# Kernel optimization log

Hardware: AMD Instinct MI355X
Metric: run time of the kernel (lower is better)

The kernel has to match this reference:

```python
import jax, jax.numpy as jnp
import numpy as np

B, N_PER_GRAPH, DEG = 4, 50000, 32
NUM_RELS, NUM_BASES, N_LAYERS = 8, 4, 2
E_PER = N_PER_GRAPH * DEG
N_TOTAL = B * N_PER_GRAPH
E_TOTAL = B * E_PER


def setup_inputs() -> dict:
    key = jax.random.key(0)
    ks = jax.random.split(key, 10)
    # Block-structured edges: each graph's edges stay within its node block (dgl.batch semantics)
    src_b = jax.random.randint(ks[0], (B, E_PER), 0, N_PER_GRAPH)
    dst_b = jax.random.randint(ks[1], (B, E_PER), 0, N_PER_GRAPH)
    off = (jnp.arange(B) * N_PER_GRAPH)[:, None]
    src = (src_b + off).reshape(-1).astype(jnp.int64)
    dst = (dst_b + off).reshape(-1).astype(jnp.int64)
    edge_type = jax.random.randint(ks[2], (E_TOTAL,), 0, NUM_RELS).astype(jnp.int64)
    norm = jax.random.uniform(ks[3], (E_TOTAL, 1), dtype=jnp.float32)
    feat1 = jax.random.normal(ks[4], (N_TOTAL, 1), dtype=jnp.float32)
    feat2 = jax.random.normal(ks[5], (N_TOTAL, 1), dtype=jnp.float32)
    # RGCN basis-decomposition params per layer (in=out=h_dim=1)
    bases = jax.random.normal(ks[6], (N_LAYERS, NUM_BASES, 1, 1), dtype=jnp.float32) * 0.1
    w_comp = jax.random.normal(ks[7], (N_LAYERS, NUM_RELS, NUM_BASES), dtype=jnp.float32) * 0.1
    biases = jnp.zeros((N_LAYERS, 1), dtype=jnp.float32)  # DGL RelGraphConv bias (out_dim=1)
    W_lin = jax.random.normal(ks[8], (1024, N_PER_GRAPH), dtype=jnp.float32) / np.float32(np.sqrt(N_PER_GRAPH))
    b_lin = jnp.zeros((1024,), dtype=jnp.float32)
    return dict(feat1=feat1, feat2=feat2, src=src, dst=dst, edge_type=edge_type,
                norm=norm, num_nodes=N_PER_GRAPH, bases=bases, w_comp=w_comp,
                biases=biases, W_lin=W_lin, b_lin=b_lin)


def _forward_each(feat, src, dst, edge_type, norm, bases, w_comp, biases, W_lin, b_lin, num_nodes):
    n_total = feat.shape[0]
    n_layers = w_comp.shape[0]
    initial = feat
    x = feat
    for l in range(n_layers):
        # basis decomposition: per-relation (1x1) weight -> scalar per relation
        weight = (w_comp[l] @ bases[l].reshape(NUM_BASES, 1))  # (num_rels, 1)
        msg = x[src] * weight[edge_type] * norm               # (E, 1) gather + edge-wise transform
        agg = jax.ops.segment_sum(msg, dst, num_segments=n_total)  # scatter-sum per node
        h = agg + biases[l]
        if l < n_layers - 1:
            h = jax.nn.relu(h)
        x = h + initial  # residual add (x += initial)
    x = x.reshape(-1, num_nodes)          # (B, num_nodes) since h_dim == 1
    return x @ W_lin.T + b_lin            # (B, 1024)


def reference(feat1, feat2, src, dst, edge_type, norm, num_nodes, bases, w_comp, biases, W_lin, b_lin):
    x1 = _forward_each(feat1, src, dst, edge_type, norm, bases, w_comp, biases, W_lin, b_lin, num_nodes)
    x2 = _forward_each(feat2, src, dst, edge_type, norm, bases, w_comp, biases, W_lin, b_lin, num_nodes)
    x = jnp.sum(x1 * x2, axis=1, keepdims=True)  # (B, 1)
    return jax.nn.sigmoid(x)
```

## Files before the change

### kernel.cpp

```cpp
#include <hip/hip_runtime.h>
#include <hip/hip_bf16.h>
#include <math.h>

#define BB 4
#define N_PER 50000
#define DEG 32
#define NUM_RELS 8
#define NUM_BASES 4
#define N_LAYERS 2
#define E_PER (N_PER * DEG)
#define E_TOTAL (BB * E_PER)
#define N_TOTAL (BB * N_PER)
#define OUT_F 1024

#define RANGES 4
#define RANGE_SZ (N_PER / RANGES)
#define SUBS 16
#define EDGES_PER_BLOCK (E_PER / SUBS)
#define GROUPS_PER_BLOCK (EDGES_PER_BLOCK / 4)
#define PARTIAL_STRIDE (2 * RANGE_SZ)
#define NBLOCKS (BB * RANGES * SUBS)

#define GR 8
#define GKSPLIT 10
#define GKCHUNK (N_PER / GKSPLIT)
#define GROWBLKS (OUT_F / GR)
#define GEMV_BLOCKS (GROWBLKS * GKSPLIT)


__global__ __launch_bounds__(256) void init_kernel(
    const float* __restrict__ feat1, const float* __restrict__ feat2,
    const float* __restrict__ bases, const float* __restrict__ w_comp,
    float* __restrict__ ws) {
  int tid = blockIdx.x * blockDim.x + threadIdx.x;
  if (blockIdx.x == 0 && threadIdx.x < 16) {
    int l = threadIdx.x >> 3, r = threadIdx.x & 7;
    float s = 0.f;
#pragma unroll
    for (int b = 0; b < NUM_BASES; ++b)
      s += w_comp[l * NUM_RELS * NUM_BASES + r * NUM_BASES + b] *
           bases[l * NUM_BASES + b];
    ws[l * 8 + r] = s;
  }
  float* x1 = ws + 32;
  float* x2 = x1 + N_TOTAL;
  for (int i = tid; i < N_TOTAL; i += gridDim.x * blockDim.x) {
    x1[i] = feat1[i];
    x2[i] = feat2[i];
  }
}

__global__ __launch_bounds__(1024) void edge_bin_kernel(
    const int* __restrict__ src, const int* __restrict__ dst,
    const int* __restrict__ et, const float* __restrict__ norm,
    const float* __restrict__ relw, int layer,
    const float* __restrict__ x1, const float* __restrict__ x2,
    float* __restrict__ partials) {
  __shared__ float w[NUM_RELS];
  __shared__ float bin1[RANGE_SZ];
  __shared__ float bin2[RANGE_SZ];
  int bid = blockIdx.x;
  int sub = bid & (SUBS - 1);
  int br = bid >> 4;
  int b = br >> 2, r = br & 3;
  if (threadIdx.x < NUM_RELS) w[threadIdx.x] = relw[layer * 8 + threadIdx.x];
  for (int i = threadIdx.x; i < RANGE_SZ; i += blockDim.x) {
    bin1[i] = 0.f;
    bin2[i] = 0.f;
  }
  __syncthreads();

  int base = b * E_PER + sub * EDGES_PER_BLOCK;
  int node_lo = b * N_PER + r * RANGE_SZ;
  for (int g = threadIdx.x; g < GROUPS_PER_BLOCK; g += blockDim.x) {
    int e = base + g * 4;
    int4 s4 = *(const int4*)(src + e);
    int4 d4 = *(const int4*)(dst + e);
    int4 t4 = *(const int4*)(et + e);
    float4 n4 = *(const float4*)(norm + e);
    {
      int lr = d4.x - node_lo;
      if (lr >= 0 && lr < RANGE_SZ) {
        float c = w[t4.x] * n4.x;
        atomicAdd(&bin1[lr], x1[s4.x] * c);
        atomicAdd(&bin2[lr], x2[s4.x] * c);
      }
    }
    {
      int lr = d4.y - node_lo;
      if (lr >= 0 && lr < RANGE_SZ) {
        float c = w[t4.y] * n4.y;
        atomicAdd(&bin1[lr], x1[s4.y] * c);
        atomicAdd(&bin2[lr], x2[s4.y] * c);
      }
    }
    {
      int lr = d4.z - node_lo;
      if (lr >= 0 && lr < RANGE_SZ) {
        float c = w[t4.z] * n4.z;
        atomicAdd(&bin1[lr], x1[s4.z] * c);
        atomicAdd(&bin2[lr], x2[s4.z] * c);
      }
    }
    {
      int lr = d4.w - node_lo;
      if (lr >= 0 && lr < RANGE_SZ) {
        float c = w[t4.w] * n4.w;
        atomicAdd(&bin1[lr], x1[s4.w] * c);
        atomicAdd(&bin2[lr], x2[s4.w] * c);
      }
    }
  }
  __syncthreads();

  float* outp = partials + (size_t)bid * PARTIAL_STRIDE;
  for (int i = threadIdx.x; i < RANGE_SZ; i += blockDim.x) {
    outp[i] = bin1[i];
    outp[RANGE_SZ + i] = bin2[i];
  }
}

__global__ __launch_bounds__(256) void merge_node_kernel(
    const float* __restrict__ partials,
    const float* __restrict__ feat1, const float* __restrict__ feat2,
    const float* __restrict__ biases, int layer,
    float* __restrict__ x1, float* __restrict__ x2) {
  int i = blockIdx.x * 256 + threadIdx.x;
  if (i >= N_TOTAL) return;
  int b = i / N_PER;
  int local = i - b * N_PER;
  int r = local / RANGE_SZ;
  int lidx = local - r * RANGE_SZ;
  int blk0 = (b * RANGES + r) * SUBS;
  float s1 = 0.f, s2 = 0.f;
#pragma unroll
  for (int s = 0; s < SUBS; ++s) {
    const float* p = partials + (size_t)(blk0 + s) * PARTIAL_STRIDE;
    s1 += p[lidx];
    s2 += p[RANGE_SZ + lidx];
  }
  float bias = biases[layer];
  float h1 = s1 + bias, h2 = s2 + bias;
  if (layer < N_LAYERS - 1) {
    h1 = fmaxf(h1, 0.f);
    h2 = fmaxf(h2, 0.f);
  }
  x1[i] = h1 + feat1[i];
  x2[i] = h2 + feat2[i];
}

__global__ __launch_bounds__(256) void gemv_part_kernel(
    const float* __restrict__ W,
    const float* __restrict__ x1, const float* __restrict__ x2,
    float* __restrict__ gpart) {
  int bid = blockIdx.x;
  int rb = bid & (GROWBLKS - 1);
  int ks = bid >> 7;
  int j0 = rb * GR;
  int k0 = ks * GKCHUNK;

  float acc[GR][8];
#pragma unroll
  for (int r = 0; r < GR; ++r)
#pragma unroll
    for (int g = 0; g < 8; ++g) acc[r][g] = 0.f;

  for (int k = k0 + threadIdx.x * 4; k < k0 + GKCHUNK; k += 256 * 4) {
    float4 xv[8];
#pragma unroll
    for (int i = 0; i < 4; ++i) {
      xv[2 * i] = *(const float4*)(x1 + i * N_PER + k);
      xv[2 * i + 1] = *(const float4*)(x2 + i * N_PER + k);
    }
#pragma unroll
    for (int r = 0; r < GR; ++r) {
      float4 wv = *(const float4*)(W + (size_t)(j0 + r) * N_PER + k);
#pragma unroll
      for (int g = 0; g < 8; ++g) {
        acc[r][g] += wv.x * xv[g].x + wv.y * xv[g].y +
                     wv.z * xv[g].z + wv.w * xv[g].w;
      }
    }
  }

#pragma unroll
  for (int off = 32; off > 0; off >>= 1)
#pragma unroll
    for (int r = 0; r < GR; ++r)
#pragma unroll
      for (int g = 0; g < 8; ++g) acc[r][g] += __shfl_down(acc[r][g], off);

  __shared__ float red[4][GR * 8];
  int wave = threadIdx.x >> 6, lane = threadIdx.x & 63;
  if (lane == 0) {
#pragma unroll
    for (int r = 0; r < GR; ++r)
#pragma unroll
      for (int g = 0; g < 8; ++g) red[wave][r * 8 + g] = acc[r][g];
  }
  __syncthreads();
  if (threadIdx.x < GR * 8) {
    float s = red[0][threadIdx.x] + red[1][threadIdx.x] +
              red[2][threadIdx.x] + red[3][threadIdx.x];
    gpart[(size_t)bid * (GR * 8) + threadIdx.x] = s;
  }
}

__global__ __launch_bounds__(1024) void gemv_reduce_kernel(
    const float* __restrict__ gpart, const float* __restrict__ b_lin,
    float* __restrict__ out) {
  int j = threadIdx.x;
  int rb = j >> 3, rr = j & 7;
  float y[8];
#pragma unroll
  for (int g = 0; g < 8; ++g) y[g] = 0.f;
#pragma unroll
  for (int ks = 0; ks < GKSPLIT; ++ks) {
    const float* p = gpart + (size_t)(ks * GROWBLKS + rb) * (GR * 8) + rr * 8;
#pragma unroll
    for (int g = 0; g < 8; ++g) y[g] += p[g];
  }
  float bl = b_lin[j];
  float prod[4];
#pragma unroll
  for (int i = 0; i < 4; ++i)
    prod[i] = (y[2 * i] + bl) * (y[2 * i + 1] + bl);

#pragma unroll
  for (int off = 32; off > 0; off >>= 1)
#pragma unroll
    for (int i = 0; i < 4; ++i) prod[i] += __shfl_down(prod[i], off);

  __shared__ float red[16][4];
  int wave = threadIdx.x >> 6, lane = threadIdx.x & 63;
  if (lane == 0) {
#pragma unroll
    for (int i = 0; i < 4; ++i) red[wave][i] = prod[i];
  }
  __syncthreads();
  if (threadIdx.x < 4) {
    float s = 0.f;
#pragma unroll
    for (int wv = 0; wv < 16; ++wv) s += red[wv][threadIdx.x];
    out[threadIdx.x] = 1.f / (1.f + expf(-s));
  }
}

extern "C" void kernel_launch(void* const* d_in, const int* in_sizes, int n_in,
                              void* d_out, int out_size, void* d_ws, size_t ws_size,
                              hipStream_t stream) {
  const float* feat1 = (const float*)d_in[0];
  const float* feat2 = (const float*)d_in[1];
  const int* src = (const int*)d_in[2];
  const int* dst = (const int*)d_in[3];
  const int* et = (const int*)d_in[4];
  const float* norm = (const float*)d_in[5];
  const float* bases = (const float*)d_in[7];
  const float* w_comp = (const float*)d_in[8];
  const float* biases = (const float*)d_in[9];
  const float* W_lin = (const float*)d_in[10];
  const float* b_lin = (const float*)d_in[11];
  float* out = (float*)d_out;

  float* ws = (float*)d_ws;
  float* relw = ws;
  float* x1 = ws + 32;
  float* x2 = x1 + N_TOTAL;
  float* partials = x2 + N_TOTAL;

  int nblk = (N_TOTAL + 255) / 256;
  init_kernel<<<nblk, 256, 0, stream>>>(feat1, feat2, bases, w_comp, ws);

  for (int l = 0; l < N_LAYERS; ++l) {
    edge_bin_kernel<<<NBLOCKS, 1024, 0, stream>>>(src, dst, et, norm, relw, l,
                                                  x1, x2, partials);
    merge_node_kernel<<<nblk, 256, 0, stream>>>(partials, feat1, feat2, biases,
                                                l, x1, x2);
  }

  float* gpart = partials;
  gemv_part_kernel<<<GEMV_BLOCKS, 256, 0, stream>>>(W_lin, x1, x2, gpart);
  gemv_reduce_kernel<<<1, 1024, 0, stream>>>(gpart, b_lin, out);
}
```

Baseline: 554.9 us.

## Interleave the two feature streams and reorder edge-bin block mapping

```diff
diff --git a/kernel.cpp b/kernel.cpp
--- a/kernel.cpp
+++ b/kernel.cpp
@@ -42,11 +42,9 @@
            bases[l * NUM_BASES + b];
     ws[l * 8 + r] = s;
   }
-  float* x1 = ws + 32;
-  float* x2 = x1 + N_TOTAL;
+  float* x12 = ws + 32;
   for (int i = tid; i < N_TOTAL; i += gridDim.x * blockDim.x) {
-    x1[i] = feat1[i];
-    x2[i] = feat2[i];
+    *(float2*)(x12 + 2 * (size_t)i) = make_float2(feat1[i], feat2[i]);
   }
 }
 
@@ -54,20 +52,16 @@
     const int* __restrict__ src, const int* __restrict__ dst,
     const int* __restrict__ et, const float* __restrict__ norm,
     const float* __restrict__ relw, int layer,
-    const float* __restrict__ x1, const float* __restrict__ x2,
-    float* __restrict__ partials) {
+    const float* __restrict__ x12, float* __restrict__ partials) {
   __shared__ float w[NUM_RELS];
-  __shared__ float bin1[RANGE_SZ];
-  __shared__ float bin2[RANGE_SZ];
+  __shared__ float bin[2 * RANGE_SZ];
   int bid = blockIdx.x;
-  int sub = bid & (SUBS - 1);
-  int br = bid >> 4;
-  int b = br >> 2, r = br & 3;
+  int r = bid >> 6;
+  int pair = bid & 63;
+  int b = pair >> 4;
+  int sub = pair & 15;
   if (threadIdx.x < NUM_RELS) w[threadIdx.x] = relw[layer * 8 + threadIdx.x];
-  for (int i = threadIdx.x; i < RANGE_SZ; i += blockDim.x) {
-    bin1[i] = 0.f;
-    bin2[i] = 0.f;
-  }
+  for (int i = threadIdx.x; i < 2 * RANGE_SZ; i += blockDim.x) bin[i] = 0.f;
   __syncthreads();
 
   int base = b * E_PER + sub * EDGES_PER_BLOCK;
@@ -80,51 +74,54 @@
     float4 n4 = *(const float4*)(norm + e);
     {
       int lr = d4.x - node_lo;
-      if (lr >= 0 && lr < RANGE_SZ) {
+      if ((unsigned)lr < RANGE_SZ) {
+        float2 xv = *(const float2*)(x12 + 2 * (size_t)s4.x);
         float c = w[t4.x] * n4.x;
-        atomicAdd(&bin1[lr], x1[s4.x] * c);
-        atomicAdd(&bin2[lr], x2[s4.x] * c);
+        atomicAdd(&bin[2 * lr], xv.x * c);
+        atomicAdd(&bin[2 * lr + 1], xv.y * c);
       }
     }
     {
       int lr = d4.y - node_lo;
-      if (lr >= 0 && lr < RANGE_SZ) {
+      if ((unsigned)lr < RANGE_SZ) {
+        float2 xv = *(const float2*)(x12 + 2 * (size_t)s4.y);
         float c = w[t4.y] * n4.y;
-        atomicAdd(&bin1[lr], x1[s4.y] * c);
-        atomicAdd(&bin2[lr], x2[s4.y] * c);
+        atomicAdd(&bin[2 * lr], xv.x * c);
+        atomicAdd(&bin[2 * lr + 1], xv.y * c);
       }
     }
     {
       int lr = d4.z - node_lo;
-      if (lr >= 0 && lr < RANGE_SZ) {
+      if ((unsigned)lr < RANGE_SZ) {
+        float2 xv = *(const float2*)(x12 + 2 * (size_t)s4.z);
         float c = w[t4.z] * n4.z;
-        atomicAdd(&bin1[lr], x1[s4.z] * c);
-        atomicAdd(&bin2[lr], x2[s4.z] * c);
+        atomicAdd(&bin[2 * lr], xv.x * c);
+        atomicAdd(&bin[2 * lr + 1], xv.y * c);
       }
     }
     {
       int lr = d4.w - node_lo;
-      if (lr >= 0 && lr < RANGE_SZ) {
+      if ((unsigned)lr < RANGE_SZ) {
+        float2 xv = *(const float2*)(x12 + 2 * (size_t)s4.w);
         float c = w[t4.w] * n4.w;
-        atomicAdd(&bin1[lr], x1[s4.w] * c);
-        atomicAdd(&bin2[lr], x2[s4.w] * c);
-      }
-    }
-  }
-  __syncthreads();
-
-  float* outp = partials + (size_t)bid * PARTIAL_STRIDE;
+        atomicAdd(&bin[2 * lr], xv.x * c);
+        atomicAdd(&bin[2 * lr + 1], xv.y * c);
+      }
+    }
+  }
+  __syncthreads();
+
+  int idx = (b * RANGES + r) * SUBS + sub;
+  float* outp = partials + (size_t)idx * PARTIAL_STRIDE;
   for (int i = threadIdx.x; i < RANGE_SZ; i += blockDim.x) {
-    outp[i] = bin1[i];
-    outp[RANGE_SZ + i] = bin2[i];
+    *(float2*)(outp + 2 * i) = make_float2(bin[2 * i], bin[2 * i + 1]);
   }
 }
 
 __global__ __launch_bounds__(256) void merge_node_kernel(
     const float* __restrict__ partials,
     const float* __restrict__ feat1, const float* __restrict__ feat2,
-    const float* __restrict__ biases, int layer,
-    float* __restrict__ x1, float* __restrict__ x2) {
+    const float* __restrict__ biases, int layer, float* __restrict__ x12) {
   int i = blockIdx.x * 256 + threadIdx.x;
   if (i >= N_TOTAL) return;
   int b = i / N_PER;
@@ -135,9 +132,10 @@
   float s1 = 0.f, s2 = 0.f;
 #pragma unroll
   for (int s = 0; s < SUBS; ++s) {
-    const float* p = partials + (size_t)(blk0 + s) * PARTIAL_STRIDE;
-    s1 += p[lidx];
-    s2 += p[RANGE_SZ + lidx];
+    float2 p = *(const float2*)(partials +
+                                (size_t)(blk0 + s) * PARTIAL_STRIDE + 2 * lidx);
+    s1 += p.x;
+    s2 += p.y;
   }
   float bias = biases[layer];
   float h1 = s1 + bias, h2 = s2 + bias;
@@ -145,13 +143,11 @@
     h1 = fmaxf(h1, 0.f);
     h2 = fmaxf(h2, 0.f);
   }
-  x1[i] = h1 + feat1[i];
-  x2[i] = h2 + feat2[i];
+  *(float2*)(x12 + 2 * (size_t)i) = make_float2(h1 + feat1[i], h2 + feat2[i]);
 }
 
 __global__ __launch_bounds__(256) void gemv_part_kernel(
-    const float* __restrict__ W,
-    const float* __restrict__ x1, const float* __restrict__ x2,
+    const float* __restrict__ W, const float* __restrict__ x12,
     float* __restrict__ gpart) {
   int bid = blockIdx.x;
   int rb = bid & (GROWBLKS - 1);
@@ -166,19 +162,22 @@
     for (int g = 0; g < 8; ++g) acc[r][g] = 0.f;
 
   for (int k = k0 + threadIdx.x * 4; k < k0 + GKCHUNK; k += 256 * 4) {
-    float4 xv[8];
+    float4 xa[4], xb[4];
 #pragma unroll
     for (int i = 0; i < 4; ++i) {
-      xv[2 * i] = *(const float4*)(x1 + i * N_PER + k);
-      xv[2 * i + 1] = *(const float4*)(x2 + i * N_PER + k);
+      const float* xg = x12 + 2 * ((size_t)i * N_PER + k);
+      xa[i] = *(const float4*)xg;
+      xb[i] = *(const float4*)(xg + 4);
     }
 #pragma unroll
     for (int r = 0; r < GR; ++r) {
       float4 wv = *(const float4*)(W + (size_t)(j0 + r) * N_PER + k);
 #pragma unroll
-      for (int g = 0; g < 8; ++g) {
-        acc[r][g] += wv.x * xv[g].x + wv.y * xv[g].y +
-                     wv.z * xv[g].z + wv.w * xv[g].w;
+      for (int i = 0; i < 4; ++i) {
+        acc[r][2 * i] +=
+            wv.x * xa[i].x + wv.y * xa[i].z + wv.z * xb[i].x + wv.w * xb[i].z;
+        acc[r][2 * i + 1] +=
+            wv.x * xa[i].y + wv.y * xa[i].w + wv.z * xb[i].y + wv.w * xb[i].w;
       }
     }
   }
@@ -264,21 +263,20 @@
 
   float* ws = (float*)d_ws;
   float* relw = ws;
-  float* x1 = ws + 32;
-  float* x2 = x1 + N_TOTAL;
-  float* partials = x2 + N_TOTAL;
+  float* x12 = ws + 32;
+  float* partials = x12 + 2 * N_TOTAL;
 
   int nblk = (N_TOTAL + 255) / 256;
   init_kernel<<<nblk, 256, 0, stream>>>(feat1, feat2, bases, w_comp, ws);
 
   for (int l = 0; l < N_LAYERS; ++l) {
     edge_bin_kernel<<<NBLOCKS, 1024, 0, stream>>>(src, dst, et, norm, relw, l,
-                                                  x1, x2, partials);
+                                                  x12, partials);
     merge_node_kernel<<<nblk, 256, 0, stream>>>(partials, feat1, feat2, biases,
-                                                l, x1, x2);
+                                                l, x12);
   }
 
   float* gpart = partials;
-  gemv_part_kernel<<<GEMV_BLOCKS, 256, 0, stream>>>(W_lin, x1, x2, gpart);
+  gemv_part_kernel<<<GEMV_BLOCKS, 256, 0, stream>>>(W_lin, x12, gpart);
   gemv_reduce_kernel<<<1, 1024, 0, stream>>>(gpart, b_lin, out);
 }
```

New measurement: 534.1 us. 3.7% less time.
